# Kernel tuning notes

Hardware: AMD Instinct MI355X
Metric: run time of the kernel (lower is better)

## Reference

```python
import jax, jax.numpy as jnp
import numpy as np

B, N, C, H = 4, 2048, 1024, 16
HD = C // H            # head dim = 64
HALF = HD // 2         # complex pairs per head = 32
VR = 32.0              # virtual_resolution
THETA = 10.0           # rope_theta


def _init_freqs():
    # mirrors init_3d_freqs_unified + per-axis replication with small noise
    rng = np.random.default_rng(0)
    idx = np.arange(HALF, dtype=np.float32)
    base = 1.0 / THETA ** (2.0 * idx / HD)                 # [HALF]
    angles = rng.uniform(0, 2 * np.pi, size=(H, 1)).astype(np.float32)
    per_head = base[None, :] * np.cos(angles)              # [H, HALF]
    freqs = np.repeat(per_head[None], 3, axis=0)           # [3, H, HALF]
    freqs = freqs + rng.normal(0, 0.01, freqs.shape).astype(np.float32)
    return jnp.asarray(freqs.reshape(3, H * HALF), dtype=jnp.float32)


def setup_inputs() -> dict:
    key = jax.random.key(0)
    ks = jax.random.split(key, 7)
    x = jax.random.normal(ks[0], (B, N, C), dtype=jnp.float32)
    t_x = jax.random.uniform(ks[1], (N,), dtype=jnp.float32)
    t_y = jax.random.uniform(ks[2], (N,), dtype=jnp.float32)
    t_z = jax.random.uniform(ks[3], (N,), dtype=jnp.float32)
    w_qkv = jax.random.normal(ks[4], (3 * C, C), dtype=jnp.float32) * (C ** -0.5)
    w_proj = jax.random.normal(ks[5], (C, C), dtype=jnp.float32) * (C ** -0.5)
    b_proj = jnp.zeros((C,), dtype=jnp.float32)
    freqs = _init_freqs()
    return {"x": x, "t_x": t_x, "t_y": t_y, "t_z": t_z,
            "w_qkv": w_qkv, "w_proj": w_proj, "b_proj": b_proj, "freqs": freqs}


def _normalize(t):
    # normalize_point_coords_3d with 'virtual_resolution'
    return (t - t.min()) / (t.max() - t.min() + 1e-8) * VR


def reference(x, t_x, t_y, t_z, w_qkv, w_proj, b_proj, freqs):
    # QKV projection (no bias)
    qkv = (x @ w_qkv.T).reshape(B, N, 3, H, HD).transpose(2, 0, 3, 1, 4)  # [3,B,H,N,HD]
    q, k, v = qkv[0], qkv[1], qkv[2]

    # mixed 3D RoPE angles: outer(t_axis, freqs[axis]) summed over axes
    tx, ty, tz = _normalize(t_x), _normalize(t_y), _normalize(t_z)
    ang = (tx[:, None] * freqs[0] + ty[:, None] * freqs[1] + tz[:, None] * freqs[2])  # [N, H*HALF]
    ang = ang.reshape(N, H, HALF).transpose(1, 0, 2)       # [H, N, HALF]
    cos, sin = jnp.cos(ang), jnp.sin(ang)

    def rotate(t):
        # complex multiply (a+ib)*(cos+isin) on even/odd pairs of last dim
        tr = t.reshape(B, H, N, HALF, 2)
        a, b = tr[..., 0], tr[..., 1]
        ra = a * cos - b * sin
        rb = a * sin + b * cos
        return jnp.stack([ra, rb], axis=-1).reshape(B, H, N, HD)

    q = rotate(q)
    k = rotate(k)

    scale = HD ** -0.5
    attn = jax.nn.softmax(jnp.einsum('bhnd,bhmd->bhnm', q * scale, k), axis=-1)
    out = jnp.einsum('bhnm,bhmd->bhnd', attn, v).transpose(0, 2, 1, 3).reshape(B, N, C)
    return out @ w_proj.T + b_proj
```

## Files before the change

### kernel.cpp

```cpp
#include <hip/hip_runtime.h>
#include <math.h>

#define BB 4
#define NN 2048
#define CC 1024
#define HH 16
#define HD 64
#define HALF 32
#define MM (BB*NN)
#define K3 (3*CC)
#define NF (HH*HALF)
#define NT (NN/64)

typedef __attribute__((ext_vector_type(8))) short bf16x8;
typedef __attribute__((ext_vector_type(4))) float f32x4;
typedef __attribute__((ext_vector_type(16))) float f32x16;
typedef __attribute__((ext_vector_type(4))) unsigned short u16x4;
typedef __attribute__((ext_vector_type(8))) unsigned short u16x8;

#define EXP2(x) exp2f(x)
#define AS1 __attribute__((address_space(1)))
#define AS3 __attribute__((address_space(3)))

__device__ __forceinline__ unsigned short f2bf(float f) {
    unsigned int u = __float_as_uint(f);
    unsigned int r = (u + 0x7FFFu + ((u >> 16) & 1u)) >> 16;
    return (unsigned short)r;
}

__global__ __launch_bounds__(256) void tnorm_kernel(const float* t_x, const float* t_y,
                                                    const float* t_z, float* tnorm) {
    int a = blockIdx.x;
    const float* t = (a == 0) ? t_x : ((a == 1) ? t_y : t_z);
    __shared__ float smn[256], smx[256];
    float mn = 1e30f, mx = -1e30f;
    for (int i = threadIdx.x; i < NN; i += 256) {
        float v = t[i];
        mn = fminf(mn, v);
        mx = fmaxf(mx, v);
    }
    smn[threadIdx.x] = mn; smx[threadIdx.x] = mx;
    __syncthreads();
    for (int s = 128; s > 0; s >>= 1) {
        if (threadIdx.x < s) {
            smn[threadIdx.x] = fminf(smn[threadIdx.x], smn[threadIdx.x + s]);
            smx[threadIdx.x] = fmaxf(smx[threadIdx.x], smx[threadIdx.x + s]);
        }
        __syncthreads();
    }
    float lo = smn[0];
    float sc = 32.0f / (smx[0] - lo + 1e-8f);
    for (int i = threadIdx.x; i < NN; i += 256)
        tnorm[a * NN + i] = (t[i] - lo) * sc;
}

__global__ __launch_bounds__(512) void angle_kernel(const float* freqs, const float* tnorm,
                                                    float* cosT, float* sinT) {
    int n = blockIdx.x;
    int hf = threadIdx.x;
    float ang = tnorm[n] * freqs[hf]
              + tnorm[NN + n] * freqs[NF + hf]
              + tnorm[2 * NN + n] * freqs[2 * NF + hf];
    cosT[(size_t)n * NF + hf] = cosf(ang);
    sinT[(size_t)n * NF + hf] = sinf(ang);
}

__global__ __launch_bounds__(256) void cvt_kernel(const float* __restrict__ src,
                                                  unsigned short* __restrict__ dst, int n) {
    int i = (blockIdx.x * 256 + threadIdx.x) * 8;
    if (i < n) {
        float4 a = *(const float4*)(src + i);
        float4 b = *(const float4*)(src + i + 4);
        u16x8 o;
        o[0] = f2bf(a.x); o[1] = f2bf(a.y); o[2] = f2bf(a.z); o[3] = f2bf(a.w);
        o[4] = f2bf(b.x); o[5] = f2bf(b.y); o[6] = f2bf(b.z); o[7] = f2bf(b.w);
        *(u16x8*)(dst + i) = o;
    }
}

__global__ __launch_bounds__(256) void qkv_gemm_kernel(const unsigned short* __restrict__ A,
                                                       const unsigned short* __restrict__ Bw,
                                                       const float* __restrict__ cosT,
                                                       const float* __restrict__ sinT,
                                                       unsigned short* __restrict__ qb,
                                                       unsigned short* __restrict__ kb,
                                                       unsigned short* __restrict__ vbT) {
    __shared__ unsigned short Asl[128 * 64];
    __shared__ unsigned short Bsl[128 * 64];
    const int tid = threadIdx.x;
    const int wv = tid >> 6, l = tid & 63;
    const int wm = wv >> 1, wn = wv & 1;
    const int lg = l >> 4, l15 = l & 15;
    const int m0 = blockIdx.x * 128, n0 = blockIdx.y * 128;

    f32x4 acc[4][4];
#pragma unroll
    for (int i = 0; i < 4; i++)
#pragma unroll
        for (int j = 0; j < 4; j++) acc[i][j] = f32x4{0.f, 0.f, 0.f, 0.f};

    for (int kt = 0; kt < CC; kt += 64) {
        __syncthreads();
#pragma unroll
        for (int i = 0; i < 4; i++) {
            int c = (wv * 4 + i) * 64 + l;
            int r = c >> 3, kc = c & 7;
            int sc = kt + ((kc ^ (r & 7)) * 8);
            __builtin_amdgcn_global_load_lds(
                (AS1 void*)(A + (size_t)(m0 + r) * CC + sc),
                (AS3 void*)(&Asl[(wv * 4 + i) * 512]), 16, 0, 0);
            __builtin_amdgcn_global_load_lds(
                (AS1 void*)(Bw + (size_t)(n0 + r) * CC + sc),
                (AS3 void*)(&Bsl[(wv * 4 + i) * 512]), 16, 0, 0);
        }
        __syncthreads();
#pragma unroll
        for (int kc = 0; kc < 2; kc++) {
            bf16x8 af[4], bfr[4];
#pragma unroll
            for (int mi = 0; mi < 4; mi++) {
                int r = wm * 64 + mi * 16 + l15;
                af[mi] = *(const bf16x8*)(&Asl[r * 64 + (((kc * 4 + lg) ^ (r & 7)) * 8)]);
            }
#pragma unroll
            for (int nj = 0; nj < 4; nj++) {
                int r = wn * 64 + nj * 16 + l15;
                bfr[nj] = *(const bf16x8*)(&Bsl[r * 64 + (((kc * 4 + lg) ^ (r & 7)) * 8)]);
            }
#pragma unroll
            for (int mi = 0; mi < 4; mi++)
#pragma unroll
                for (int nj = 0; nj < 4; nj++)
                    acc[mi][nj] = __builtin_amdgcn_mfma_f32_16x16x32_bf16(af[mi], bfr[nj], acc[mi][nj], 0, 0, 0);
        }
    }
    const int b_ = m0 >> 11;
    const int nrow0 = (m0 & (NN - 1));
#pragma unroll
    for (int nj = 0; nj < 4; nj++) {
        int oc = n0 + wn * 64 + nj * 16 + l15;
        int s = oc >> 10;
        int rr = oc & 1023;
        int h = rr >> 6;
        int d = rr & 63;
        int f = d >> 1;
#pragma unroll
        for (int mi = 0; mi < 4; mi++) {
            f32x4 v = acc[mi][nj];
            if (s == 2) {
                u16x4 vv;
#pragma unroll
                for (int reg = 0; reg < 4; reg++) vv[reg] = f2bf(v[reg]);
                int nb = nrow0 + wm * 64 + mi * 16 + lg * 4;
                *(u16x4*)(vbT + ((size_t)((b_ * HH + h) * HD + d)) * NN + nb) = vv;
            } else {
#pragma unroll
                for (int reg = 0; reg < 4; reg++) {
                    int m = m0 + wm * 64 + mi * 16 + lg * 4 + reg;
                    int n = m & (NN - 1);
                    float val = v[reg];
                    float partner = __shfl_xor(val, 1);
                    size_t base = (((size_t)(b_ * HH + h)) * NN + n) * HD + d;
                    float cs = cosT[(size_t)n * NF + h * HALF + f];
                    float sn = sinT[(size_t)n * NF + h * HALF + f];
                    float res = ((d & 1) == 0) ? (val * cs - partner * sn)
                                               : (val * cs + partner * sn);
                    if (s == 0) res *= 0.18033688011112043f;
                    (s == 0 ? qb : kb)[base] = f2bf(res);
                }
            }
        }
    }
}

__global__ __launch_bounds__(256, 2) void attn_mfma_kernel(const unsigned short* __restrict__ qbp,
                                                           const unsigned short* __restrict__ kbp,
                                                           const unsigned short* __restrict__ vtp,
                                                           unsigned short* __restrict__ aout) {
    __shared__ unsigned short Ks[2][64 * 64];
    __shared__ unsigned short Vts[2][64 * 64];
    const int tid = threadIdx.x;
    const int wv = tid >> 6;
    const int l = tid & 63;
    const int l31 = l & 31, hi = l >> 5;

    const int wg = blockIdx.x;
    const int Lidx = (wg & 7) * 64 + (wg >> 3);
    const int bh = Lidx >> 3;
    const int q0 = (Lidx & 7) * 256;

    const unsigned short* qp = qbp + (size_t)bh * (NN * HD);
    const unsigned short* kp = kbp + (size_t)bh * (NN * HD);
    const unsigned short* vp = vtp + (size_t)bh * (NN * HD);

    const int r0 = (wv * 2 + 0) * 8 + (l >> 3);
    const int r1 = (wv * 2 + 1) * 8 + (l >> 3);
    const int c0 = ((l & 7) ^ (r0 & 7)) * 8;
    const int c1 = ((l & 7) ^ (r1 & 7)) * 8;
    const unsigned short* ksrc0 = kp + r0 * HD + c0;
    const unsigned short* ksrc1 = kp + r1 * HD + c1;
    const unsigned short* vsrc0 = vp + (size_t)r0 * NN + c0;
    const unsigned short* vsrc1 = vp + (size_t)r1 * NN + c1;

#define STAGE(buf, kt) do { \
    __builtin_amdgcn_global_load_lds((AS1 void*)(ksrc0 + (kt) * 4096), (AS3 void*)(&Ks[buf][(wv * 2 + 0) * 512]), 16, 0, 0); \
    __builtin_amdgcn_global_load_lds((AS1 void*)(ksrc1 + (kt) * 4096), (AS3 void*)(&Ks[buf][(wv * 2 + 1) * 512]), 16, 0, 0); \
    __builtin_amdgcn_global_load_lds((AS1 void*)(vsrc0 + (kt) * 64),   (AS3 void*)(&Vts[buf][(wv * 2 + 0) * 512]), 16, 0, 0); \
    __builtin_amdgcn_global_load_lds((AS1 void*)(vsrc1 + (kt) * 64),   (AS3 void*)(&Vts[buf][(wv * 2 + 1) * 512]), 16, 0, 0); \
} while (0)

    STAGE(0, 0);

    const unsigned short* qr = qp + (size_t)(q0 + wv * 64 + l31) * HD;
    bf16x8 qfA[4], qfB[4];
#pragma unroll
    for (int dc = 0; dc < 4; dc++) {
        qfA[dc] = *(const bf16x8*)(qr + dc * 16 + hi * 8);
        qfB[dc] = *(const bf16x8*)(qr + 32 * HD + dc * 16 + hi * 8);
    }

    int so[4];
#pragma unroll
    for (int i = 0; i < 4; i++) so[i] = ((2 * i + hi) ^ (l31 & 7)) * 8;

    float lA = 0.0f, lB = 0.0f;
    f32x16 OA0, OA1, OB0, OB1;
#pragma unroll
    for (int r = 0; r < 16; r++) { OA0[r] = 0.f; OA1[r] = 0.f; OB0[r] = 0.f; OB1[r] = 0.f; }

    __syncthreads();

    int cur = 0;
    for (int kt = 0; kt < NT; kt++) {
        if (kt + 1 < NT) STAGE(cur ^ 1, kt + 1);

        const unsigned short* kb_ = &Ks[cur][0];
        const unsigned short* vb_ = &Vts[cur][0];

        f32x16 sA0, sA1, sB0, sB1;
#pragma unroll
        for (int r = 0; r < 16; r++) { sA0[r] = 0.f; sA1[r] = 0.f; sB0[r] = 0.f; sB1[r] = 0.f; }
        __builtin_amdgcn_s_setprio(1);
#pragma unroll
        for (int dc = 0; dc < 4; dc++) {
            bf16x8 a0 = *(const bf16x8*)(kb_ + l31 * 64 + so[dc]);
            bf16x8 a1 = *(const bf16x8*)(kb_ + (32 + l31) * 64 + so[dc]);
            sA0 = __builtin_amdgcn_mfma_f32_32x32x16_bf16(a0, qfA[dc], sA0, 0, 0, 0);
            sA1 = __builtin_amdgcn_mfma_f32_32x32x16_bf16(a1, qfA[dc], sA1, 0, 0, 0);
            sB0 = __builtin_amdgcn_mfma_f32_32x32x16_bf16(a0, qfB[dc], sB0, 0, 0, 0);
            sB1 = __builtin_amdgcn_mfma_f32_32x32x16_bf16(a1, qfB[dc], sB1, 0, 0, 0);
        }
        __builtin_amdgcn_s_setprio(0);

        float sumA, sumB;
        {
            float sa = 0.f, sb = 0.f;
#pragma unroll
            for (int r = 0; r < 16; r++) {
                sA0[r] = EXP2(sA0[r]); sa += sA0[r];
                sA1[r] = EXP2(sA1[r]); sb += sA1[r];
            }
            sumA = sa + sb;
            sa = 0.f; sb = 0.f;
#pragma unroll
            for (int r = 0; r < 16; r++) {
                sB0[r] = EXP2(sB0[r]); sa += sB0[r];
                sB1[r] = EXP2(sB1[r]); sb += sB1[r];
            }
            sumB = sa + sb;
        }
#pragma unroll
        for (int r = 0; r < 8; r++) {
            unsigned u0, u1, u2, u3;
            asm("v_cvt_pk_bf16_f32 %0, %1, %2" : "=v"(u0) : "v"(sA0[2 * r]), "v"(sA0[2 * r + 1]));
            asm("v_cvt_pk_bf16_f32 %0, %1, %2" : "=v"(u1) : "v"(sA1[2 * r]), "v"(sA1[2 * r + 1]));
            asm("v_cvt_pk_bf16_f32 %0, %1, %2" : "=v"(u2) : "v"(sB0[2 * r]), "v"(sB0[2 * r + 1]));
            asm("v_cvt_pk_bf16_f32 %0, %1, %2" : "=v"(u3) : "v"(sB1[2 * r]), "v"(sB1[2 * r + 1]));
            sA0[2 * r] = __uint_as_float(u0);
            sA1[2 * r] = __uint_as_float(u1);
            sB0[2 * r] = __uint_as_float(u2);
            sB1[2 * r] = __uint_as_float(u3);
        }
        sumA += __shfl_xor(sumA, 32);
        sumB += __shfl_xor(sumB, 32);
        lA += sumA;
        lB += sumB;

        __builtin_amdgcn_s_setprio(1);
#pragma unroll
        for (int kc = 0; kc < 4; kc++) {
            const int bs = (kc & 1) * 8;
            union { unsigned u[4]; bf16x8 v; } pfA, pfB;
            {
                float e0 = (kc < 2) ? sA0[bs + 0] : sA1[bs + 0];
                float e4 = (kc < 2) ? sA0[bs + 4] : sA1[bs + 4];
                float e2 = (kc < 2) ? sA0[bs + 2] : sA1[bs + 2];
                float e6 = (kc < 2) ? sA0[bs + 6] : sA1[bs + 6];
                auto uA = __builtin_amdgcn_permlane32_swap(__float_as_uint(e0), __float_as_uint(e4), false, false);
                auto uB = __builtin_amdgcn_permlane32_swap(__float_as_uint(e2), __float_as_uint(e6), false, false);
                pfA.u[0] = uA[0]; pfA.u[1] = uB[0]; pfA.u[2] = uA[1]; pfA.u[3] = uB[1];
            }
            {
                float e0 = (kc < 2) ? sB0[bs + 0] : sB1[bs + 0];
                float e4 = (kc < 2) ? sB0[bs + 4] : sB1[bs + 4];
                float e2 = (kc < 2) ? sB0[bs + 2] : sB1[bs + 2];
                float e6 = (kc < 2) ? sB0[bs + 6] : sB1[bs + 6];
                auto uA = __builtin_amdgcn_permlane32_swap(__float_as_uint(e0), __float_as_uint(e4), false, false);
                auto uB = __builtin_amdgcn_permlane32_swap(__float_as_uint(e2), __float_as_uint(e6), false, false);
                pfB.u[0] = uA[0]; pfB.u[1] = uB[0]; pfB.u[2] = uA[1]; pfB.u[3] = uB[1];
            }
            bf16x8 va  = *(const bf16x8*)(vb_ + l31 * 64 + so[kc]);
            bf16x8 vb2 = *(const bf16x8*)(vb_ + (32 + l31) * 64 + so[kc]);
            OA0 = __builtin_amdgcn_mfma_f32_32x32x16_bf16(va,  pfA.v, OA0, 0, 0, 0);
            OA1 = __builtin_amdgcn_mfma_f32_32x32x16_bf16(vb2, pfA.v, OA1, 0, 0, 0);
            OB0 = __builtin_amdgcn_mfma_f32_32x32x16_bf16(va,  pfB.v, OB0, 0, 0, 0);
            OB1 = __builtin_amdgcn_mfma_f32_32x32x16_bf16(vb2, pfB.v, OB1, 0, 0, 0);
        }
        __builtin_amdgcn_s_setprio(0);
        __syncthreads();
        cur ^= 1;
    }

    const int b_ = bh >> 4, hh = bh & 15;
    const float invA = 1.0f / lA, invB = 1.0f / lB;
    const size_t mrowA = (size_t)(b_ * NN + q0 + wv * 64 + l31) * CC + hh * HD;
    const size_t mrowB = mrowA + (size_t)32 * CC;
#pragma unroll
    for (int rq = 0; rq < 4; rq++) {
        u16x4 a0, a1, b0, b1;
#pragma unroll
        for (int j = 0; j < 4; j++) {
            a0[j] = f2bf(OA0[rq * 4 + j] * invA);
            a1[j] = f2bf(OA1[rq * 4 + j] * invA);
            b0[j] = f2bf(OB0[rq * 4 + j] * invB);
            b1[j] = f2bf(OB1[rq * 4 + j] * invB);
        }
        *(u16x4*)(aout + mrowA + rq * 8 + hi * 4) = a0;
        *(u16x4*)(aout + mrowA + 32 + rq * 8 + hi * 4) = a1;
        *(u16x4*)(aout + mrowB + rq * 8 + hi * 4) = b0;
        *(u16x4*)(aout + mrowB + 32 + rq * 8 + hi * 4) = b1;
    }
#undef STAGE
}

__global__ __launch_bounds__(256) void proj_gemm_kernel(const unsigned short* __restrict__ A,
                                                        const unsigned short* __restrict__ Bw,
                                                        const float* __restrict__ bp,
                                                        float* __restrict__ out) {
    __shared__ unsigned short Asl[128 * 64];
    __shared__ unsigned short Bsl[128 * 64];
    const int tid = threadIdx.x;
    const int wv = tid >> 6, l = tid & 63;
    const int wm = wv >> 1, wn = wv & 1;
    const int lg = l >> 4, l15 = l & 15;
    const int m0 = blockIdx.x * 128, n0 = blockIdx.y * 128;

    f32x4 acc[4][4];
#pragma unroll
    for (int i = 0; i < 4; i++)
#pragma unroll
        for (int j = 0; j < 4; j++) acc[i][j] = f32x4{0.f, 0.f, 0.f, 0.f};

    for (int kt = 0; kt < CC; kt += 64) {
        __syncthreads();
#pragma unroll
        for (int i = 0; i < 4; i++) {
            int c = (wv * 4 + i) * 64 + l;
            int r = c >> 3, kc = c & 7;
            int sc = kt + ((kc ^ (r & 7)) * 8);
            __builtin_amdgcn_global_load_lds(
                (AS1 void*)(A + (size_t)(m0 + r) * CC + sc),
                (AS3 void*)(&Asl[(wv * 4 + i) * 512]), 16, 0, 0);
            __builtin_amdgcn_global_load_lds(
                (AS1 void*)(Bw + (size_t)(n0 + r) * CC + sc),
                (AS3 void*)(&Bsl[(wv * 4 + i) * 512]), 16, 0, 0);
        }
        __syncthreads();
#pragma unroll
        for (int kc = 0; kc < 2; kc++) {
            bf16x8 af[4], bfr[4];
#pragma unroll
            for (int mi = 0; mi < 4; mi++) {
                int r = wm * 64 + mi * 16 + l15;
                af[mi] = *(const bf16x8*)(&Asl[r * 64 + (((kc * 4 + lg) ^ (r & 7)) * 8)]);
            }
#pragma unroll
            for (int nj = 0; nj < 4; nj++) {
                int r = wn * 64 + nj * 16 + l15;
                bfr[nj] = *(const bf16x8*)(&Bsl[r * 64 + (((kc * 4 + lg) ^ (r & 7)) * 8)]);
            }
#pragma unroll
            for (int mi = 0; mi < 4; mi++)
#pragma unroll
                for (int nj = 0; nj < 4; nj++)
                    acc[mi][nj] = __builtin_amdgcn_mfma_f32_16x16x32_bf16(af[mi], bfr[nj], acc[mi][nj], 0, 0, 0);
        }
    }
    float bias[4];
#pragma unroll
    for (int nj = 0; nj < 4; nj++) bias[nj] = bp[n0 + wn * 64 + nj * 16 + l15];
#pragma unroll
    for (int mi = 0; mi < 4; mi++)
#pragma unroll
        for (int nj = 0; nj < 4; nj++) {
            int oc = n0 + wn * 64 + nj * 16 + l15;
#pragma unroll
            for (int reg = 0; reg < 4; reg++) {
                int m = m0 + wm * 64 + mi * 16 + lg * 4 + reg;
                out[(size_t)m * CC + oc] = acc[mi][nj][reg] + bias[nj];
            }
        }
}

extern "C" void kernel_launch(void* const* d_in, const int* in_sizes, int n_in,
                              void* d_out, int out_size, void* d_ws, size_t ws_size,
                              hipStream_t stream) {
    const float* x      = (const float*)d_in[0];
    const float* t_x    = (const float*)d_in[1];
    const float* t_y    = (const float*)d_in[2];
    const float* t_z    = (const float*)d_in[3];
    const float* w_qkv  = (const float*)d_in[4];
    const float* w_proj = (const float*)d_in[5];
    const float* b_proj = (const float*)d_in[6];
    const float* freqs  = (const float*)d_in[7];
    float* out = (float*)d_out;

    unsigned short* xb     = (unsigned short*)d_ws;
    unsigned short* wqkvb  = xb + (size_t)MM * CC;
    unsigned short* wprojb = wqkvb + (size_t)K3 * CC;
    unsigned short* qbuf   = wprojb + (size_t)CC * CC;
    unsigned short* kbuf   = qbuf + (size_t)BB * HH * NN * HD;
    unsigned short* vbT    = kbuf + (size_t)BB * HH * NN * HD;
    unsigned short* attnb  = vbT + (size_t)BB * HH * NN * HD;
    float* cosT  = (float*)(attnb + (size_t)MM * CC);
    float* sinT  = cosT + (size_t)NN * NF;
    float* tnorm = sinT + (size_t)NN * NF;

    tnorm_kernel<<<3, 256, 0, stream>>>(t_x, t_y, t_z, tnorm);
    angle_kernel<<<NN, 512, 0, stream>>>(freqs, tnorm, cosT, sinT);
    cvt_kernel<<<(MM * CC) / 2048, 256, 0, stream>>>(x, xb, MM * CC);
    cvt_kernel<<<(K3 * CC) / 2048, 256, 0, stream>>>(w_qkv, wqkvb, K3 * CC);
    cvt_kernel<<<(CC * CC) / 2048, 256, 0, stream>>>(w_proj, wprojb, CC * CC);
    qkv_gemm_kernel<<<dim3(MM / 128, K3 / 128), 256, 0, stream>>>(xb, wqkvb, cosT, sinT,
                                                                  qbuf, kbuf, vbT);
    attn_mfma_kernel<<<512, 256, 0, stream>>>(qbuf, kbuf, vbT, attnb);
    proj_gemm_kernel<<<dim3(MM / 128, CC / 128), 256, 0, stream>>>(attnb, wprojb, b_proj, out);
}
```

Baseline: 235.3 us.

## Compute softmax row sums via MFMA with ones and unroll double buffer

Replaces the per-lane VALU accumulation of exp sums and the cross-lane shuffle with two extra MFMAs that multiply a ones matrix by the bf16 probabilities, so the row sums build up in accumulator registers. The K-tile loop is unrolled by two through a templated iteration function so buffer indices are compile-time constants and LDS pointers are advanced incrementally. The first score MFMA starts from a zero operand and exp2 uses the hardware builtin. The sums now come from bf16-rounded probabilities, which matches the values fed to PV. The cost is two more MFMAs per sub-step and more accumulator registers.

```diff
diff --git a/kernel.cpp b/kernel.cpp
--- a/kernel.cpp
+++ b/kernel.cpp
@@ -17,8 +17,13 @@
 typedef __attribute__((ext_vector_type(16))) float f32x16;
 typedef __attribute__((ext_vector_type(4))) unsigned short u16x4;
 typedef __attribute__((ext_vector_type(8))) unsigned short u16x8;
-
+typedef __attribute__((ext_vector_type(4))) unsigned int u32x4;
+
+#if __has_builtin(__builtin_amdgcn_exp2f)
+#define EXP2(x) __builtin_amdgcn_exp2f(x)
+#else
 #define EXP2(x) exp2f(x)
+#endif
 #define AS1 __attribute__((address_space(1)))
 #define AS3 __attribute__((address_space(3)))
 
@@ -173,12 +178,103 @@
     }
 }
 
+template<int BUF>
+__device__ __forceinline__ void attn_iter(
+    unsigned short* LB, bool do_stage, int wv, int l31,
+    const unsigned short*& kn0, const unsigned short*& kn1,
+    const unsigned short*& vn0, const unsigned short*& vn1,
+    const int (&so)[4], const bf16x8 (&qfA)[4], const bf16x8 (&qfB)[4],
+    const f32x16& Z, const bf16x8& ones,
+    f32x16& OA0, f32x16& OA1, f32x16& OB0, f32x16& OB1,
+    f32x16& SsA, f32x16& SsB) {
+    if (do_stage) {
+        const int nb = (BUF ^ 1) * 4096;
+        __builtin_amdgcn_global_load_lds((AS1 void*)kn0, (AS3 void*)(&LB[nb + (wv * 2 + 0) * 512]), 16, 0, 0);
+        __builtin_amdgcn_global_load_lds((AS1 void*)kn1, (AS3 void*)(&LB[nb + (wv * 2 + 1) * 512]), 16, 0, 0);
+        __builtin_amdgcn_global_load_lds((AS1 void*)vn0, (AS3 void*)(&LB[8192 + nb + (wv * 2 + 0) * 512]), 16, 0, 0);
+        __builtin_amdgcn_global_load_lds((AS1 void*)vn1, (AS3 void*)(&LB[8192 + nb + (wv * 2 + 1) * 512]), 16, 0, 0);
+        kn0 += 4096; kn1 += 4096; vn0 += 64; vn1 += 64;
+    }
+    f32x16 sA0, sA1, sB0, sB1;
+    __builtin_amdgcn_s_setprio(1);
+    {
+        bf16x8 a0 = *(const bf16x8*)(LB + BUF * 4096 + l31 * 64 + so[0]);
+        bf16x8 a1 = *(const bf16x8*)(LB + BUF * 4096 + (32 + l31) * 64 + so[0]);
+        sA0 = __builtin_amdgcn_mfma_f32_32x32x16_bf16(a0, qfA[0], Z, 0, 0, 0);
+        sA1 = __builtin_amdgcn_mfma_f32_32x32x16_bf16(a1, qfA[0], Z, 0, 0, 0);
+        sB0 = __builtin_amdgcn_mfma_f32_32x32x16_bf16(a0, qfB[0], Z, 0, 0, 0);
+        sB1 = __builtin_amdgcn_mfma_f32_32x32x16_bf16(a1, qfB[0], Z, 0, 0, 0);
+    }
+#pragma unroll
+    for (int dc = 1; dc < 4; dc++) {
+        bf16x8 a0 = *(const bf16x8*)(LB + BUF * 4096 + l31 * 64 + so[dc]);
+        bf16x8 a1 = *(const bf16x8*)(LB + BUF * 4096 + (32 + l31) * 64 + so[dc]);
+        sA0 = __builtin_amdgcn_mfma_f32_32x32x16_bf16(a0, qfA[dc], sA0, 0, 0, 0);
+        sA1 = __builtin_amdgcn_mfma_f32_32x32x16_bf16(a1, qfA[dc], sA1, 0, 0, 0);
+        sB0 = __builtin_amdgcn_mfma_f32_32x32x16_bf16(a0, qfB[dc], sB0, 0, 0, 0);
+        sB1 = __builtin_amdgcn_mfma_f32_32x32x16_bf16(a1, qfB[dc], sB1, 0, 0, 0);
+    }
+    __builtin_amdgcn_s_setprio(0);
+#pragma unroll
+    for (int r = 0; r < 16; r++) {
+        sA0[r] = EXP2(sA0[r]); sA1[r] = EXP2(sA1[r]);
+        sB0[r] = EXP2(sB0[r]); sB1[r] = EXP2(sB1[r]);
+    }
+#pragma unroll
+    for (int r = 0; r < 8; r++) {
+        unsigned u0, u1, u2, u3;
+        asm("v_cvt_pk_bf16_f32 %0, %1, %2" : "=v"(u0) : "v"(sA0[2 * r]), "v"(sA0[2 * r + 1]));
+        asm("v_cvt_pk_bf16_f32 %0, %1, %2" : "=v"(u1) : "v"(sA1[2 * r]), "v"(sA1[2 * r + 1]));
+        asm("v_cvt_pk_bf16_f32 %0, %1, %2" : "=v"(u2) : "v"(sB0[2 * r]), "v"(sB0[2 * r + 1]));
+        asm("v_cvt_pk_bf16_f32 %0, %1, %2" : "=v"(u3) : "v"(sB1[2 * r]), "v"(sB1[2 * r + 1]));
+        sA0[2 * r] = __uint_as_float(u0);
+        sA1[2 * r] = __uint_as_float(u1);
+        sB0[2 * r] = __uint_as_float(u2);
+        sB1[2 * r] = __uint_as_float(u3);
+    }
+    __builtin_amdgcn_s_setprio(1);
+#pragma unroll
+    for (int kc = 0; kc < 4; kc++) {
+        const int bs = (kc & 1) * 8;
+        bf16x8 pfA, pfB;
+        {
+            float e0 = (kc < 2) ? sA0[bs + 0] : sA1[bs + 0];
+            float e4 = (kc < 2) ? sA0[bs + 4] : sA1[bs + 4];
+            float e2 = (kc < 2) ? sA0[bs + 2] : sA1[bs + 2];
+            float e6 = (kc < 2) ? sA0[bs + 6] : sA1[bs + 6];
+            auto uA = __builtin_amdgcn_permlane32_swap(__float_as_uint(e0), __float_as_uint(e4), false, false);
+            auto uB = __builtin_amdgcn_permlane32_swap(__float_as_uint(e2), __float_as_uint(e6), false, false);
+            u32x4 t; t.x = uA[0]; t.y = uB[0]; t.z = uA[1]; t.w = uB[1];
+            pfA = __builtin_bit_cast(bf16x8, t);
+        }
+        {
+            float e0 = (kc < 2) ? sB0[bs + 0] : sB1[bs + 0];
+            float e4 = (kc < 2) ? sB0[bs + 4] : sB1[bs + 4];
+            float e2 = (kc < 2) ? sB0[bs + 2] : sB1[bs + 2];
+            float e6 = (kc < 2) ? sB0[bs + 6] : sB1[bs + 6];
+            auto uA = __builtin_amdgcn_permlane32_swap(__float_as_uint(e0), __float_as_uint(e4), false, false);
+            auto uB = __builtin_amdgcn_permlane32_swap(__float_as_uint(e2), __float_as_uint(e6), false, false);
+            u32x4 t; t.x = uA[0]; t.y = uB[0]; t.z = uA[1]; t.w = uB[1];
+            pfB = __builtin_bit_cast(bf16x8, t);
+        }
+        bf16x8 va  = *(const bf16x8*)(LB + 8192 + BUF * 4096 + l31 * 64 + so[kc]);
+        bf16x8 vb2 = *(const bf16x8*)(LB + 8192 + BUF * 4096 + (32 + l31) * 64 + so[kc]);
+        OA0 = __builtin_amdgcn_mfma_f32_32x32x16_bf16(va,  pfA, OA0, 0, 0, 0);
+        OA1 = __builtin_amdgcn_mfma_f32_32x32x16_bf16(vb2, pfA, OA1, 0, 0, 0);
+        OB0 = __builtin_amdgcn_mfma_f32_32x32x16_bf16(va,  pfB, OB0, 0, 0, 0);
+        OB1 = __builtin_amdgcn_mfma_f32_32x32x16_bf16(vb2, pfB, OB1, 0, 0, 0);
+        SsA = __builtin_amdgcn_mfma_f32_32x32x16_bf16(ones, pfA, SsA, 0, 0, 0);
+        SsB = __builtin_amdgcn_mfma_f32_32x32x16_bf16(ones, pfB, SsB, 0, 0, 0);
+    }
+    __builtin_amdgcn_s_setprio(0);
+    __syncthreads();
+}
+
 __global__ __launch_bounds__(256, 2) void attn_mfma_kernel(const unsigned short* __restrict__ qbp,
                                                            const unsigned short* __restrict__ kbp,
                                                            const unsigned short* __restrict__ vtp,
                                                            unsigned short* __restrict__ aout) {
-    __shared__ unsigned short Ks[2][64 * 64];
-    __shared__ unsigned short Vts[2][64 * 64];
+    __shared__ unsigned short LB[4 * 4096];
     const int tid = threadIdx.x;
     const int wv = tid >> 6;
     const int l = tid & 63;
@@ -197,19 +293,16 @@
     const int r1 = (wv * 2 + 1) * 8 + (l >> 3);
     const int c0 = ((l & 7) ^ (r0 & 7)) * 8;
     const int c1 = ((l & 7) ^ (r1 & 7)) * 8;
-    const unsigned short* ksrc0 = kp + r0 * HD + c0;
-    const unsigned short* ksrc1 = kp + r1 * HD + c1;
-    const unsigned short* vsrc0 = vp + (size_t)r0 * NN + c0;
-    const unsigned short* vsrc1 = vp + (size_t)r1 * NN + c1;
-
-#define STAGE(buf, kt) do { \
-    __builtin_amdgcn_global_load_lds((AS1 void*)(ksrc0 + (kt) * 4096), (AS3 void*)(&Ks[buf][(wv * 2 + 0) * 512]), 16, 0, 0); \
-    __builtin_amdgcn_global_load_lds((AS1 void*)(ksrc1 + (kt) * 4096), (AS3 void*)(&Ks[buf][(wv * 2 + 1) * 512]), 16, 0, 0); \
-    __builtin_amdgcn_global_load_lds((AS1 void*)(vsrc0 + (kt) * 64),   (AS3 void*)(&Vts[buf][(wv * 2 + 0) * 512]), 16, 0, 0); \
-    __builtin_amdgcn_global_load_lds((AS1 void*)(vsrc1 + (kt) * 64),   (AS3 void*)(&Vts[buf][(wv * 2 + 1) * 512]), 16, 0, 0); \
-} while (0)
-
-    STAGE(0, 0);
+    const unsigned short* kn0 = kp + r0 * HD + c0;
+    const unsigned short* kn1 = kp + r1 * HD + c1;
+    const unsigned short* vn0 = vp + (size_t)r0 * NN + c0;
+    const unsigned short* vn1 = vp + (size_t)r1 * NN + c1;
+
+    __builtin_amdgcn_global_load_lds((AS1 void*)kn0, (AS3 void*)(&LB[(wv * 2 + 0) * 512]), 16, 0, 0);
+    __builtin_amdgcn_global_load_lds((AS1 void*)kn1, (AS3 void*)(&LB[(wv * 2 + 1) * 512]), 16, 0, 0);
+    __builtin_amdgcn_global_load_lds((AS1 void*)vn0, (AS3 void*)(&LB[8192 + (wv * 2 + 0) * 512]), 16, 0, 0);
+    __builtin_amdgcn_global_load_lds((AS1 void*)vn1, (AS3 void*)(&LB[8192 + (wv * 2 + 1) * 512]), 16, 0, 0);
+    kn0 += 4096; kn1 += 4096; vn0 += 64; vn1 += 64;
 
     const unsigned short* qr = qp + (size_t)(q0 + wv * 64 + l31) * HD;
     bf16x8 qfA[4], qfB[4];
@@ -223,106 +316,25 @@
 #pragma unroll
     for (int i = 0; i < 4; i++) so[i] = ((2 * i + hi) ^ (l31 & 7)) * 8;
 
-    float lA = 0.0f, lB = 0.0f;
-    f32x16 OA0, OA1, OB0, OB1;
-#pragma unroll
-    for (int r = 0; r < 16; r++) { OA0[r] = 0.f; OA1[r] = 0.f; OB0[r] = 0.f; OB1[r] = 0.f; }
+    f32x16 Z;
+#pragma unroll
+    for (int r = 0; r < 16; r++) Z[r] = 0.0f;
+    f32x16 OA0 = Z, OA1 = Z, OB0 = Z, OB1 = Z, SsA = Z, SsB = Z;
+    bf16x8 ones;
+#pragma unroll
+    for (int j = 0; j < 8; j++) ones[j] = (short)0x3F80;
 
     __syncthreads();
 
-    int cur = 0;
-    for (int kt = 0; kt < NT; kt++) {
-        if (kt + 1 < NT) STAGE(cur ^ 1, kt + 1);
-
-        const unsigned short* kb_ = &Ks[cur][0];
-        const unsigned short* vb_ = &Vts[cur][0];
-
-        f32x16 sA0, sA1, sB0, sB1;
-#pragma unroll
-        for (int r = 0; r < 16; r++) { sA0[r] = 0.f; sA1[r] = 0.f; sB0[r] = 0.f; sB1[r] = 0.f; }
-        __builtin_amdgcn_s_setprio(1);
-#pragma unroll
-        for (int dc = 0; dc < 4; dc++) {
-            bf16x8 a0 = *(const bf16x8*)(kb_ + l31 * 64 + so[dc]);
-            bf16x8 a1 = *(const bf16x8*)(kb_ + (32 + l31) * 64 + so[dc]);
-            sA0 = __builtin_amdgcn_mfma_f32_32x32x16_bf16(a0, qfA[dc], sA0, 0, 0, 0);
-            sA1 = __builtin_amdgcn_mfma_f32_32x32x16_bf16(a1, qfA[dc], sA1, 0, 0, 0);
-            sB0 = __builtin_amdgcn_mfma_f32_32x32x16_bf16(a0, qfB[dc], sB0, 0, 0, 0);
-            sB1 = __builtin_amdgcn_mfma_f32_32x32x16_bf16(a1, qfB[dc], sB1, 0, 0, 0);
-        }
-        __builtin_amdgcn_s_setprio(0);
-
-        float sumA, sumB;
-        {
-            float sa = 0.f, sb = 0.f;
-#pragma unroll
-            for (int r = 0; r < 16; r++) {
-                sA0[r] = EXP2(sA0[r]); sa += sA0[r];
-                sA1[r] = EXP2(sA1[r]); sb += sA1[r];
-            }
-            sumA = sa + sb;
-            sa = 0.f; sb = 0.f;
-#pragma unroll
-            for (int r = 0; r < 16; r++) {
-                sB0[r] = EXP2(sB0[r]); sa += sB0[r];
-                sB1[r] = EXP2(sB1[r]); sb += sB1[r];
-            }
-            sumB = sa + sb;
-        }
-#pragma unroll
-        for (int r = 0; r < 8; r++) {
-            unsigned u0, u1, u2, u3;
-            asm("v_cvt_pk_bf16_f32 %0, %1, %2" : "=v"(u0) : "v"(sA0[2 * r]), "v"(sA0[2 * r + 1]));
-            asm("v_cvt_pk_bf16_f32 %0, %1, %2" : "=v"(u1) : "v"(sA1[2 * r]), "v"(sA1[2 * r + 1]));
-            asm("v_cvt_pk_bf16_f32 %0, %1, %2" : "=v"(u2) : "v"(sB0[2 * r]), "v"(sB0[2 * r + 1]));
-            asm("v_cvt_pk_bf16_f32 %0, %1, %2" : "=v"(u3) : "v"(sB1[2 * r]), "v"(sB1[2 * r + 1]));
-            sA0[2 * r] = __uint_as_float(u0);
-            sA1[2 * r] = __uint_as_float(u1);
-            sB0[2 * r] = __uint_as_float(u2);
-            sB1[2 * r] = __uint_as_float(u3);
-        }
-        sumA += __shfl_xor(sumA, 32);
-        sumB += __shfl_xor(sumB, 32);
-        lA += sumA;
-        lB += sumB;
-
-        __builtin_amdgcn_s_setprio(1);
-#pragma unroll
-        for (int kc = 0; kc < 4; kc++) {
-            const int bs = (kc & 1) * 8;
-            union { unsigned u[4]; bf16x8 v; } pfA, pfB;
-            {
-                float e0 = (kc < 2) ? sA0[bs + 0] : sA1[bs + 0];
-                float e4 = (kc < 2) ? sA0[bs + 4] : sA1[bs + 4];
-                float e2 = (kc < 2) ? sA0[bs + 2] : sA1[bs + 2];
-                float e6 = (kc < 2) ? sA0[bs + 6] : sA1[bs + 6];
-                auto uA = __builtin_amdgcn_permlane32_swap(__float_as_uint(e0), __float_as_uint(e4), false, false);
-                auto uB = __builtin_amdgcn_permlane32_swap(__float_as_uint(e2), __float_as_uint(e6), false, false);
-                pfA.u[0] = uA[0]; pfA.u[1] = uB[0]; pfA.u[2] = uA[1]; pfA.u[3] = uB[1];
-            }
-            {
-                float e0 = (kc < 2) ? sB0[bs + 0] : sB1[bs + 0];
-                float e4 = (kc < 2) ? sB0[bs + 4] : sB1[bs + 4];
-                float e2 = (kc < 2) ? sB0[bs + 2] : sB1[bs + 2];
-                float e6 = (kc < 2) ? sB0[bs + 6] : sB1[bs + 6];
-                auto uA = __builtin_amdgcn_permlane32_swap(__float_as_uint(e0), __float_as_uint(e4), false, false);
-                auto uB = __builtin_amdgcn_permlane32_swap(__float_as_uint(e2), __float_as_uint(e6), false, false);
-                pfB.u[0] = uA[0]; pfB.u[1] = uB[0]; pfB.u[2] = uA[1]; pfB.u[3] = uB[1];
-            }
-            bf16x8 va  = *(const bf16x8*)(vb_ + l31 * 64 + so[kc]);
-            bf16x8 vb2 = *(const bf16x8*)(vb_ + (32 + l31) * 64 + so[kc]);
-            OA0 = __builtin_amdgcn_mfma_f32_32x32x16_bf16(va,  pfA.v, OA0, 0, 0, 0);
-            OA1 = __builtin_amdgcn_mfma_f32_32x32x16_bf16(vb2, pfA.v, OA1, 0, 0, 0);
-            OB0 = __builtin_amdgcn_mfma_f32_32x32x16_bf16(va,  pfB.v, OB0, 0, 0, 0);
-            OB1 = __builtin_amdgcn_mfma_f32_32x32x16_bf16(vb2, pfB.v, OB1, 0, 0, 0);
-        }
-        __builtin_amdgcn_s_setprio(0);
-        __syncthreads();
-        cur ^= 1;
+    for (int ktb = 0; ktb < NT; ktb += 2) {
+        attn_iter<0>(LB, true, wv, l31, kn0, kn1, vn0, vn1, so, qfA, qfB,
+                     Z, ones, OA0, OA1, OB0, OB1, SsA, SsB);
+        attn_iter<1>(LB, ktb + 2 < NT, wv, l31, kn0, kn1, vn0, vn1, so, qfA, qfB,
+                     Z, ones, OA0, OA1, OB0, OB1, SsA, SsB);
     }
 
     const int b_ = bh >> 4, hh = bh & 15;
-    const float invA = 1.0f / lA, invB = 1.0f / lB;
+    const float invA = 1.0f / SsA[0], invB = 1.0f / SsB[0];
     const size_t mrowA = (size_t)(b_ * NN + q0 + wv * 64 + l31) * CC + hh * HD;
     const size_t mrowB = mrowA + (size_t)32 * CC;
 #pragma unroll
@@ -340,7 +352,6 @@
         *(u16x4*)(aout + mrowB + rq * 8 + hi * 4) = b0;
         *(u16x4*)(aout + mrowB + 32 + rq * 8 + hi * 4) = b1;
     }
-#undef STAGE
 }
 
 __global__ __launch_bounds__(256) void proj_gemm_kernel(const unsigned short* __restrict__ A,
```

After: 210.4 us. 10.6% less time.
